# Optimization experiments

Hardware: AMD Instinct MI355X
Metric: run time of the kernel (lower is better)

The kernel has to match this reference:

```python
import jax, jax.numpy as jnp
import numpy as np

N_NODES = 100000
N_EDGES = 1000000
F_DIM = 128


def setup_inputs() -> dict:
    key = jax.random.key(0)
    ks = jax.random.split(key, 12)
    s = lambda k, shape: jax.random.normal(k, shape, dtype=jnp.float32) * (1.0 / np.sqrt(shape[0]))
    return {
        "x": jax.random.normal(ks[0], (N_NODES, F_DIM), dtype=jnp.float32),
        "edge_index": jax.random.randint(ks[1], (2, N_EDGES), 0, N_NODES, dtype=jnp.int64),
        "W1": s(ks[2], (2 * F_DIM, 64)), "b1": jnp.zeros((64,), jnp.float32), "A1": s(ks[3], (2 * F_DIM, 64)),
        "W2": s(ks[4], (64, 32)), "b2": jnp.zeros((32,), jnp.float32), "A2": s(ks[5], (64, 32)),
        "W3": s(ks[6], (32, 16)), "b3": jnp.zeros((16,), jnp.float32), "A3": s(ks[7], (32, 16)),
        "Wf": s(ks[8], (16, 1)), "bf": jnp.zeros((1,), jnp.float32),
    }


def _res_block(h, W, b, A):
    # out = relu(h @ W + b); residual = h @ A (bias-free adjust); return relu(out + residual)
    out = jax.nn.relu(h @ W + b)
    return jax.nn.relu(out + h @ A)


def reference(x, edge_index, W1, b1, A1, W2, b2, A2, W3, b3, A3, Wf, bf):
    # NOTE: in the original forward, the GNN output is overwritten by data.x,
    # so the effective computation is gather -> concat -> residual MLP -> sigmoid.
    src, dst = edge_index[0], edge_index[1]
    h = jnp.concatenate([x[src], x[dst]], axis=-1)  # [E, 2F]
    h = _res_block(h, W1, b1, A1)  # [E, 64]
    h = _res_block(h, W2, b2, A2)  # [E, 32]
    h = _res_block(h, W3, b3, A3)  # [E, 16]
    return jax.nn.sigmoid(h @ Wf + bf)  # [E, 1]
```

## Files before the change

kernel.cpp:

```cpp
#include <hip/hip_runtime.h>
#include <stdint.h>
#include <stddef.h>

#define E_TOTAL 1000000
#define N_NODES 100000
#define FD      128
#define ETILE   64
#define NTILES  (E_TOTAL / ETILE)
#define GRID    2048

typedef __attribute__((ext_vector_type(8))) short short8;
typedef __attribute__((ext_vector_type(4))) short short4v;
typedef __attribute__((ext_vector_type(4))) float f32x4;

__device__ __forceinline__ short f2bf(float f) {
  union { float f; unsigned u; } v; v.f = f;
  unsigned r = (v.u + 0x7FFFu + ((v.u >> 16) & 1u)) >> 16;
  return (short)(r & 0xFFFFu);
}

__device__ __forceinline__ int h0idx(int row, int c) {
  return row * 256 + (c ^ ((row & 7) << 3));
}
__device__ __forceinline__ int h1idx(int row, int c) {
  return row * 64 + (c ^ (((row >> 1) & 7) << 3));
}

__global__ __launch_bounds__(256, 2)
void linkpred_kernel(const float* __restrict__ x,
                     const int* __restrict__ ei,
                     const float* __restrict__ W1, const float* __restrict__ b1,
                     const float* __restrict__ A1,
                     const float* __restrict__ W2, const float* __restrict__ b2,
                     const float* __restrict__ A2,
                     const float* __restrict__ W3, const float* __restrict__ b3,
                     const float* __restrict__ A3,
                     const float* __restrict__ Wf, const float* __restrict__ bfp,
                     float* __restrict__ out)
{
  __shared__ __align__(16) short H0[ETILE * 256];
  __shared__ __align__(16) short H12[ETILE * 64];

  const int tid  = threadIdx.x;
  const int w    = tid >> 6;
  const int lane = tid & 63;
  const int col  = lane & 15;
  const int quad = lane >> 4;

  short8 B1f[2][8];
  for (int p = 0; p < 2; ++p) {
    const int n = 16 * (w + 4 * p) + col;
    const float* src = (p == 0) ? (W1 + n) : (A1 + (n - 64));
    for (int kt = 0; kt < 8; ++kt) {
      short8 f;
      for (int j = 0; j < 8; ++j)
        f[j] = f2bf(src[(kt * 32 + quad * 8 + j) * 64]);
      B1f[p][kt] = f;
    }
  }
  short8 B2f[2][2];
  for (int p = 0; p < 2; ++p) {
    const int n = 16 * ((w & 1) + 2 * p) + col;
    const float* src = (p == 0) ? (W2 + n) : (A2 + (n - 32));
    for (int kt = 0; kt < 2; ++kt) {
      short8 f;
      for (int j = 0; j < 8; ++j)
        f[j] = f2bf(src[(kt * 32 + quad * 8 + j) * 32]);
      B2f[p][kt] = f;
    }
  }
  short8 B3f[2];
  for (int p = 0; p < 2; ++p) {
    const int n = 16 * p + col;
    const float* src = (p == 0) ? (W3 + n) : (A3 + (n - 16));
    short8 f;
    for (int j = 0; j < 8; ++j)
      f[j] = f2bf(src[(quad * 8 + j) * 16]);
    B3f[p] = f;
  }
  const float b1v = b1[16 * w + col];
  const float b2v = b2[16 * (w & 1) + col];
  const float b3v = b3[col];
  const float bfv = bfp[0];
  const float Wfv = Wf[col];
  const f32x4 zero = {0.f, 0.f, 0.f, 0.f};

  const int half = lane >> 5;
  const int cc   = lane & 31;

  for (int tile = blockIdx.x; tile < NTILES; tile += gridDim.x) {
    const int e0 = tile * ETILE;

    int nd[16];
#pragma unroll
    for (int it = 0; it < 16; ++it)
      nd[it] = ei[half * E_TOTAL + e0 + it * 4 + w];
#pragma unroll
    for (int it = 0; it < 16; ++it) {
      const int e = it * 4 + w;
      const float4 v = ((const float4*)(x + (size_t)nd[it] * FD))[cc];
      short4v s4;
      s4[0] = f2bf(v.x); s4[1] = f2bf(v.y); s4[2] = f2bf(v.z); s4[3] = f2bf(v.w);
      *(short4v*)&H0[h0idx(e, half * 128 + cc * 4)] = s4;
    }
    __syncthreads();

    for (int mt = 0; mt < 4; ++mt) {
      f32x4 a0 = zero, a1 = zero;
      for (int kt = 0; kt < 8; ++kt) {
        short8 a = *(const short8*)&H0[h0idx(mt * 16 + col, kt * 32 + quad * 8)];
        a0 = __builtin_amdgcn_mfma_f32_16x16x32_bf16(a, B1f[0][kt], a0, 0, 0, 0);
        a1 = __builtin_amdgcn_mfma_f32_16x16x32_bf16(a, B1f[1][kt], a1, 0, 0, 0);
      }
      for (int r = 0; r < 4; ++r) {
        float o = fmaxf(a0[r] + b1v, 0.f);
        float h = fmaxf(o + a1[r], 0.f);
        H12[h1idx(mt * 16 + quad * 4 + r, 16 * w + col)] = f2bf(h);
      }
    }
    __syncthreads();

    f32x4 c2w[2], c2a[2];
    c2w[0] = zero; c2w[1] = zero; c2a[0] = zero; c2a[1] = zero;
    for (int mi = 0; mi < 2; ++mi) {
      const int m = (2 * (w >> 1) + mi) * 16 + col;
      for (int kt = 0; kt < 2; ++kt) {
        short8 a = *(const short8*)&H12[h1idx(m, kt * 32 + quad * 8)];
        c2w[mi] = __builtin_amdgcn_mfma_f32_16x16x32_bf16(a, B2f[0][kt], c2w[mi], 0, 0, 0);
        c2a[mi] = __builtin_amdgcn_mfma_f32_16x16x32_bf16(a, B2f[1][kt], c2a[mi], 0, 0, 0);
      }
    }
    __syncthreads();

    for (int mi = 0; mi < 2; ++mi)
      for (int r = 0; r < 4; ++r) {
        float o = fmaxf(c2w[mi][r] + b2v, 0.f);
        float h = fmaxf(o + c2a[mi][r], 0.f);
        H12[((2 * (w >> 1) + mi) * 16 + quad * 4 + r) * 40 + 16 * (w & 1) + col] = f2bf(h);
      }
    __syncthreads();

    f32x4 acc3[2];
    acc3[0] = zero; acc3[1] = zero;
    {
      short8 a = *(const short8*)&H12[(w * 16 + col) * 40 + quad * 8];
      acc3[0] = __builtin_amdgcn_mfma_f32_16x16x32_bf16(a, B3f[0], acc3[0], 0, 0, 0);
      acc3[1] = __builtin_amdgcn_mfma_f32_16x16x32_bf16(a, B3f[1], acc3[1], 0, 0, 0);
    }

#pragma unroll
    for (int r = 0; r < 4; ++r) {
      float o = fmaxf(acc3[0][r] + b3v, 0.f);
      float h = fmaxf(o + acc3[1][r], 0.f);
      float t = h * Wfv;
      t += __shfl_xor(t, 1, 16);
      t += __shfl_xor(t, 2, 16);
      t += __shfl_xor(t, 4, 16);
      t += __shfl_xor(t, 8, 16);
      if (col == r) {
        float s = bfv + t;
        out[e0 + w * 16 + quad * 4 + r] = 1.0f / (1.0f + __expf(-s));
      }
    }
  }
}

extern "C" void kernel_launch(void* const* d_in, const int* in_sizes, int n_in,
                              void* d_out, int out_size, void* d_ws, size_t ws_size,
                              hipStream_t stream) {
  const float* x   = (const float*)d_in[0];
  const int*   ei  = (const int*)d_in[1];
  const float* W1  = (const float*)d_in[2];
  const float* b1  = (const float*)d_in[3];
  const float* A1  = (const float*)d_in[4];
  const float* W2  = (const float*)d_in[5];
  const float* b2  = (const float*)d_in[6];
  const float* A2  = (const float*)d_in[7];
  const float* W3  = (const float*)d_in[8];
  const float* b3  = (const float*)d_in[9];
  const float* A3  = (const float*)d_in[10];
  const float* Wf  = (const float*)d_in[11];
  const float* bfp = (const float*)d_in[12];

  hipLaunchKernelGGL(linkpred_kernel, dim3(GRID), dim3(256), 0, stream,
                     x, ei, W1, b1, A1, W2, b2, A2, W3, b3, A3, Wf, bfp,
                     (float*)d_out);
}
```

Baseline: 252.7 us.

## Pre-convert node features to bf16 in workspace before gather kernel

Adds a conversion kernel that writes x as bf16 into the workspace once per call, so the main kernel gathers 256-byte rows instead of 512-byte fp32 rows and skips per-edge conversion. The gather is remapped to 16-byte short8 loads per lane. Grid size is halved from 2048 to 1024. The cost is an extra launch and a full pass over x (51MB read, 25MB write), and the fp32 path remains only as a fallback when workspace is too small.

```diff
diff --git a/kernel.cpp b/kernel.cpp
--- a/kernel.cpp
+++ b/kernel.cpp
@@ -7,7 +7,7 @@
 #define FD      128
 #define ETILE   64
 #define NTILES  (E_TOTAL / ETILE)
-#define GRID    2048
+#define GRID    1024
 
 typedef __attribute__((ext_vector_type(8))) short short8;
 typedef __attribute__((ext_vector_type(4))) short short4v;
@@ -26,8 +26,23 @@
   return row * 64 + (c ^ (((row >> 1) & 7) << 3));
 }
 
+__global__ __launch_bounds__(256)
+void cvt_kernel(const float* __restrict__ x, short* __restrict__ xb) {
+  const int total = N_NODES * FD / 8;
+  for (int i = blockIdx.x * 256 + threadIdx.x; i < total; i += gridDim.x * 256) {
+    float4 a = ((const float4*)x)[2 * i];
+    float4 b = ((const float4*)x)[2 * i + 1];
+    short8 s;
+    s[0] = f2bf(a.x); s[1] = f2bf(a.y); s[2] = f2bf(a.z); s[3] = f2bf(a.w);
+    s[4] = f2bf(b.x); s[5] = f2bf(b.y); s[6] = f2bf(b.z); s[7] = f2bf(b.w);
+    ((short8*)xb)[i] = s;
+  }
+}
+
+template <int USEBF>
 __global__ __launch_bounds__(256, 2)
 void linkpred_kernel(const float* __restrict__ x,
+                     const short* __restrict__ xb,
                      const int* __restrict__ ei,
                      const float* __restrict__ W1, const float* __restrict__ b1,
                      const float* __restrict__ A1,
@@ -85,23 +100,38 @@
   const float Wfv = Wf[col];
   const f32x4 zero = {0.f, 0.f, 0.f, 0.f};
 
-  const int half = lane >> 5;
-  const int cc   = lane & 31;
+  const int half32 = lane >> 5;
+  const int cc     = lane & 31;
 
   for (int tile = blockIdx.x; tile < NTILES; tile += gridDim.x) {
     const int e0 = tile * ETILE;
 
-    int nd[16];
-#pragma unroll
-    for (int it = 0; it < 16; ++it)
-      nd[it] = ei[half * E_TOTAL + e0 + it * 4 + w];
-#pragma unroll
-    for (int it = 0; it < 16; ++it) {
-      const int e = it * 4 + w;
-      const float4 v = ((const float4*)(x + (size_t)nd[it] * FD))[cc];
-      short4v s4;
-      s4[0] = f2bf(v.x); s4[1] = f2bf(v.y); s4[2] = f2bf(v.z); s4[3] = f2bf(v.w);
-      *(short4v*)&H0[h0idx(e, half * 128 + cc * 4)] = s4;
+    if (USEBF) {
+      int nd[8];
+#pragma unroll
+      for (int it = 0; it < 8; ++it) {
+        const int e = it * 8 + 2 * w + (quad >> 1);
+        nd[it] = ei[(quad & 1) * E_TOTAL + e0 + e];
+      }
+#pragma unroll
+      for (int it = 0; it < 8; ++it) {
+        const int e = it * 8 + 2 * w + (quad >> 1);
+        short8 s = *(const short8*)(xb + (size_t)nd[it] * FD + col * 8);
+        *(short8*)&H0[h0idx(e, (quad & 1) * 128 + col * 8)] = s;
+      }
+    } else {
+      int nd[16];
+#pragma unroll
+      for (int it = 0; it < 16; ++it)
+        nd[it] = ei[half32 * E_TOTAL + e0 + it * 4 + w];
+#pragma unroll
+      for (int it = 0; it < 16; ++it) {
+        const int e = it * 4 + w;
+        const float4 v = ((const float4*)(x + (size_t)nd[it] * FD))[cc];
+        short4v s4;
+        s4[0] = f2bf(v.x); s4[1] = f2bf(v.y); s4[2] = f2bf(v.z); s4[3] = f2bf(v.w);
+        *(short4v*)&H0[h0idx(e, half32 * 128 + cc * 4)] = s4;
+      }
     }
     __syncthreads();
 
@@ -182,7 +212,17 @@
   const float* Wf  = (const float*)d_in[11];
   const float* bfp = (const float*)d_in[12];
 
-  hipLaunchKernelGGL(linkpred_kernel, dim3(GRID), dim3(256), 0, stream,
-                     x, ei, W1, b1, A1, W2, b2, A2, W3, b3, A3, Wf, bfp,
-                     (float*)d_out);
-}
+  short* xb = (short*)d_ws;
+  const size_t need = (size_t)N_NODES * FD * sizeof(short);
+
+  if (ws_size >= need) {
+    hipLaunchKernelGGL(cvt_kernel, dim3(2048), dim3(256), 0, stream, x, xb);
+    hipLaunchKernelGGL(HIP_KERNEL_NAME(linkpred_kernel<1>), dim3(GRID), dim3(256), 0, stream,
+                       x, (const short*)xb, ei, W1, b1, A1, W2, b2, A2, W3, b3, A3,
+                       Wf, bfp, (float*)d_out);
+  } else {
+    hipLaunchKernelGGL(HIP_KERNEL_NAME(linkpred_kernel<0>), dim3(GRID), dim3(256), 0, stream,
+                       x, (const short*)nullptr, ei, W1, b1, A1, W2, b2, A2, W3, b3, A3,
+                       Wf, bfp, (float*)d_out);
+  }
+}
```

New measurement: 290.3 us. 14.9% more time.
